# Kernel optimization log

Hardware: AMD Instinct MI355X
Metric: run time of the kernel (lower is better)

Reference implementation:

```python
import jax, jax.numpy as jnp
import numpy as np

D_MODEL = 512
NHEAD = 8
HEAD_DIM = D_MODEL // NHEAD
SEQ = 4096
BATCH = 2
BASE = 10000.0


def rope_cache(seq_len, dim):
    inv_freq = 1.0 / (BASE ** (jnp.arange(0, dim, 2, dtype=jnp.float32) / dim))
    t = jnp.arange(seq_len, dtype=jnp.float32)
    freqs = jnp.einsum('i,j->ij', t, inv_freq)          # [S, dim/2]
    emb = jnp.concatenate([freqs, freqs], axis=-1)       # [S, dim]
    return jnp.cos(emb), jnp.sin(emb)


def rotate_half(x):
    h = x.shape[-1] // 2
    return jnp.concatenate([-x[..., h:], x[..., :h]], axis=-1)


def setup_inputs() -> dict:
    key = jax.random.key(0)
    ks = jax.random.split(key, 9)
    s = 1.0 / np.sqrt(D_MODEL)
    x = jax.random.normal(ks[0], (BATCH, SEQ, D_MODEL), dtype=jnp.float32)
    Wq = jax.random.uniform(ks[1], (D_MODEL, D_MODEL), jnp.float32, -s, s)
    bq = jax.random.uniform(ks[2], (D_MODEL,), jnp.float32, -s, s)
    Wk = jax.random.uniform(ks[3], (D_MODEL, D_MODEL), jnp.float32, -s, s)
    bk = jax.random.uniform(ks[4], (D_MODEL,), jnp.float32, -s, s)
    Wv = jax.random.uniform(ks[5], (D_MODEL, D_MODEL), jnp.float32, -s, s)
    bv = jax.random.uniform(ks[6], (D_MODEL,), jnp.float32, -s, s)
    Wo = jax.random.uniform(ks[7], (D_MODEL, D_MODEL), jnp.float32, -s, s)
    bo = jax.random.uniform(ks[8], (D_MODEL,), jnp.float32, -s, s)
    # causal mask: True where attention is disallowed (j > i)
    mask = jnp.triu(jnp.ones((SEQ, SEQ), dtype=bool), k=1)
    return {"x": x, "mask": mask, "Wq": Wq, "bq": bq, "Wk": Wk, "bk": bk,
            "Wv": Wv, "bv": bv, "Wo": Wo, "bo": bo}


def reference(x, mask, Wq, bq, Wk, bk, Wv, bv, Wo, bo):
    B, S, _ = x.shape
    def proj(W, b):
        y = x @ W.T + b
        return y.reshape(B, S, NHEAD, HEAD_DIM).transpose(0, 2, 1, 3)  # [B,H,S,D]
    q = proj(Wq, bq)
    k = proj(Wk, bk)
    v = proj(Wv, bv)
    cos, sin = rope_cache(S, HEAD_DIM)                    # [S, D]
    cos = cos[None, None]; sin = sin[None, None]
    q = q * cos + rotate_half(q) * sin
    k = k * cos + rotate_half(k) * sin
    scale = HEAD_DIM ** -0.5
    attn = jnp.einsum('bhid,bhjd->bhij', q, k) * scale    # [B,H,S,S]
    attn = jnp.where(mask[None, None], -jnp.inf, attn)
    attn = jax.nn.softmax(attn, axis=-1)
    out = jnp.einsum('bhij,bhjd->bhid', attn, v)          # [B,H,S,D]
    out = out.transpose(0, 2, 1, 3).reshape(B, S, D_MODEL)
    return out @ Wo.T + bo
```

## Files before the change

kernel.cpp:

```cpp
#include <hip/hip_runtime.h>
#include <hip/hip_bf16.h>

#define SEQLEN 4096
#define DMODEL 512
#define NHEADS 8

typedef short short8 __attribute__((ext_vector_type(8)));
typedef float f32x4  __attribute__((ext_vector_type(4)));
typedef float f32x16 __attribute__((ext_vector_type(16)));
typedef int   int2v  __attribute__((ext_vector_type(2)));

__device__ __forceinline__ unsigned short f2bf(float f) {
    union { float f; unsigned u; } v; v.f = f;
    unsigned r = v.u + 0x7fffu + ((v.u >> 16) & 1u);
    return (unsigned short)(r >> 16);
}
__device__ __forceinline__ float bf2f(unsigned short u) {
    union { unsigned u; float f; } v; v.u = (unsigned)u << 16; return v.f;
}
__device__ __forceinline__ float exp2v(float x) {
    float r; asm("v_exp_f32 %0, %1" : "=v"(r) : "v"(x)); return r;
}
__device__ __forceinline__ unsigned cvtpk(float lo, float hi) {
    unsigned r; asm("v_cvt_pk_bf16_f32 %0, %1, %2" : "=v"(r) : "v"(lo), "v"(hi)); return r;
}
__device__ __forceinline__ int2v pl32(int a, int b) {
    return __builtin_amdgcn_permlane32_swap(a, b, false, false);
}
__device__ __forceinline__ void gload16(const void* g, void* l) {
    __builtin_amdgcn_global_load_lds(
        (const __attribute__((address_space(1))) void*)g,
        (__attribute__((address_space(3))) void*)l, 16, 0, 0);
}

__global__ __launch_bounds__(256)
void prep_kernel(const float* __restrict__ x,
                 const float* __restrict__ Wq, const float* __restrict__ Wk,
                 const float* __restrict__ Wv, const float* __restrict__ Wo,
                 unsigned short* __restrict__ xb, unsigned short* __restrict__ Wcat,
                 float* __restrict__ ct, float* __restrict__ st) {
    const int gid = blockIdx.x, tid = threadIdx.x;
    if (gid < 4096) {
        int i = gid * 1024 + tid * 4;
        float4 v = *reinterpret_cast<const float4*>(x + i);
        ushort4 o; o.x = f2bf(v.x); o.y = f2bf(v.y); o.z = f2bf(v.z); o.w = f2bf(v.w);
        *reinterpret_cast<ushort4*>(xb + i) = o;
    } else if (gid < 5120) {
        int i = (gid - 4096) * 1024 + tid * 4;
        int z = i >> 18;
        const float* W = (z == 0) ? Wq : (z == 1) ? Wk : (z == 2) ? Wv : Wo;
        int j = i & 262143;
        float4 v = *reinterpret_cast<const float4*>(W + j);
        ushort4 o; o.x = f2bf(v.x); o.y = f2bf(v.y); o.z = f2bf(v.z); o.w = f2bf(v.w);
        *reinterpret_cast<ushort4*>(Wcat + i) = o;
    } else {
        int idx = (gid - 5120) * 256 + tid;
        int s = idx >> 5, f = idx & 31;
        float inv = powf(10000.0f, -(float)f * (1.0f / 32.0f));
        float a = (float)s * inv;
        ct[idx] = cosf(a); st[idx] = sinf(a);
    }
}

template<int MODE>
__global__ __launch_bounds__(256)
void gemm_kernel(const unsigned short* __restrict__ A,
                 const unsigned short* __restrict__ W,
                 const float* __restrict__ bq,
                 const float* __restrict__ bk,
                 const float* __restrict__ bv,
                 const float* __restrict__ ctab,
                 const float* __restrict__ stab,
                 unsigned short* __restrict__ Qb,
                 unsigned short* __restrict__ Kb,
                 unsigned short* __restrict__ Vt,
                 float* __restrict__ Fout)
{
    constexpr int K = 512;
    constexpr int NT = (MODE == 0) ? 12 : 4;
    constexpr int CPX = (MODE == 0) ? 96 : 32;
    __shared__ __align__(16) unsigned short smem[3][2][128 * 32];

    const int raw = blockIdx.x;
    const int bid = (raw & 7) * CPX + (raw >> 3);
    const int bm = bid / NT, bn = bid % NT;
    const int tid = threadIdx.x;
    const int w = tid >> 6, l = tid & 63;
    const int g = l >> 4, l15 = l & 15;
    const int wr = w >> 1, wc = w & 1;

    const int sr0 = tid >> 2;
    const int swzc = (tid & 3) ^ ((sr0 >> 1) & 3);
    const unsigned wbase = (unsigned)(tid & 0xC0) * 16;
    const unsigned short* arow = A + (size_t)(bm * 128 + sr0) * K + swzc * 8;
    const unsigned short* brow = W + (size_t)(bn * 128 + sr0) * K + swzc * 8;

    f32x4 acc[4][4];
    #pragma unroll
    for (int p = 0; p < 4; ++p)
        #pragma unroll
        for (int q = 0; q < 4; ++q)
            acc[p][q] = (f32x4){0.f, 0.f, 0.f, 0.f};

    auto stage = [&](int buf, int k0) {
        char* ab = (char*)smem[buf][0];
        char* bb2 = (char*)smem[buf][1];
        gload16(arow + k0,                      ab + wbase);
        gload16(arow + (size_t)64 * K + k0,     ab + 4096 + wbase);
        gload16(brow + k0,                      bb2 + wbase);
        gload16(brow + (size_t)64 * K + k0,     bb2 + 4096 + wbase);
    };

    stage(0, 0);
    stage(1, 32);
    asm volatile("s_waitcnt vmcnt(4)" ::: "memory");
    __builtin_amdgcn_s_barrier();

    int cb = 0;
    for (int ks = 0; ks < 16; ++ks) {
        int pb = cb + 2; if (pb >= 3) pb -= 3;
        stage(pb, (ks + 2 < 16) ? (ks + 2) * 32 : 480);

        const char* ab = (const char*)smem[cb][0];
        const char* bb2 = (const char*)smem[cb][1];
        short8 af[4], bf[4];
        #pragma unroll
        for (int mt = 0; mt < 4; ++mt) {
            int r = wr * 64 + mt * 16 + l15;
            int ofs = (r * 64 + g * 16) ^ (((r >> 1) & 3) << 4);
            af[mt] = *reinterpret_cast<const short8*>(ab + ofs);
        }
        #pragma unroll
        for (int nt = 0; nt < 4; ++nt) {
            int r = wc * 64 + nt * 16 + l15;
            int ofs = (r * 64 + g * 16) ^ (((r >> 1) & 3) << 4);
            bf[nt] = *reinterpret_cast<const short8*>(bb2 + ofs);
        }
        __builtin_amdgcn_s_setprio(1);
        #pragma unroll
        for (int mt = 0; mt < 4; ++mt)
            #pragma unroll
            for (int nt = 0; nt < 4; ++nt)
                acc[mt][nt] = __builtin_amdgcn_mfma_f32_16x16x32_bf16(af[mt], bf[nt], acc[mt][nt], 0, 0, 0);
        __builtin_amdgcn_s_setprio(0);

        asm volatile("s_waitcnt vmcnt(4)" ::: "memory");
        __builtin_amdgcn_s_barrier();
        cb = (cb == 2) ? 0 : cb + 1;
    }

    const int m_base = bm * 128 + wr * 64;

    if (MODE == 1) {
        const int n_base = bn * 128 + wc * 64;
        #pragma unroll
        for (int mt = 0; mt < 4; ++mt)
            for (int nt = 0; nt < 4; ++nt) {
                int n = n_base + nt * 16 + l15;
                float bb = bq[n];
                #pragma unroll
                for (int i = 0; i < 4; ++i) {
                    int m = m_base + mt * 16 + g * 4 + i;
                    Fout[(size_t)m * 512 + n] = acc[mt][nt][i] + bb;
                }
            }
    } else {
        const int z = bn >> 2;
        const int nc0 = (bn & 3) * 128 + wc * 64;
        const float* bias = (z == 0) ? bq : (z == 1) ? bk : bv;
        if (z < 2) {
            unsigned short* Y = z ? Kb : Qb;
            const float qsc = z ? 1.0f : 0.18033688011112042f;
            #pragma unroll
            for (int mt = 0; mt < 4; ++mt)
                for (int ntl = 0; ntl < 2; ++ntl) {
                    int hd0 = (ntl * 16 + l15) & 31;
                    int n0 = nc0 + ntl * 16 + l15;
                    float bb0 = bias[n0];
                    float bb1 = bias[n0 + 32];
                    #pragma unroll
                    for (int i = 0; i < 4; ++i) {
                        int m = m_base + mt * 16 + g * 4 + i;
                        int sidx = m & (SEQLEN - 1);
                        float cs = ctab[sidx * 32 + hd0];
                        float sn = stab[sidx * 32 + hd0];
                        float v0 = acc[mt][ntl][i] + bb0;
                        float v1 = acc[mt][ntl + 2][i] + bb1;
                        Y[(size_t)m * 512 + n0]      = f2bf((v0 * cs - v1 * sn) * qsc);
                        Y[(size_t)m * 512 + n0 + 32] = f2bf((v1 * cs + v0 * sn) * qsc);
                    }
                }
        } else {
            asm volatile("s_waitcnt vmcnt(0)" ::: "memory");
            __builtin_amdgcn_s_barrier();
            char* T = (char*)smem;
            #pragma unroll
            for (int mt = 0; mt < 4; ++mt)
                #pragma unroll
                for (int nt = 0; nt < 4; ++nt) {
                    int nv_l = wc * 64 + nt * 16 + l15;
                    float bb = bias[(bn & 3) * 128 + nv_l];
                    #pragma unroll
                    for (int i = 0; i < 4; i += 2) {
                        int m_l = wr * 64 + mt * 16 + g * 4 + i;
                        unsigned u = cvtpk(acc[mt][nt][i] + bb, acc[mt][nt][i + 1] + bb);
                        int byte0 = nv_l * 256 + ((m_l * 2) ^ ((nv_l & 7) << 4));
                        *reinterpret_cast<unsigned*>(T + byte0) = u;
                    }
                }
            __builtin_amdgcn_s_barrier();
            const int b_out = bm >> 5;
            const int s0 = (bm & 31) * 128;
            #pragma unroll
            for (int p = 0; p < 8; ++p) {
                int nv_l = p * 16 + (tid >> 4);
                int c = tid & 15;
                int byte = nv_l * 256 + ((c * 16) ^ ((nv_l & 7) << 4));
                short8 v = *reinterpret_cast<const short8*>(T + byte);
                int nv_g = (bn & 3) * 128 + nv_l;
                int hg = nv_g >> 6, d = nv_g & 63;
                *reinterpret_cast<short8*>(
                    Vt + ((size_t)((b_out * 8 + hg) * 64 + d)) * SEQLEN + s0 + c * 8) = v;
            }
        }
    }
}

template<int SPLIT>
__global__ __launch_bounds__(256, 2)
void attn_kernel(const unsigned short* __restrict__ Qg,
                 const unsigned short* __restrict__ Kg,
                 const unsigned short* __restrict__ Vt,
                 unsigned short* __restrict__ O,
                 unsigned short* __restrict__ Opt,
                 float* __restrict__ Ml)
{
    __shared__ __align__(16) unsigned short k_sh[3][64 * 64];
    __shared__ __align__(16) unsigned short v_sh[3][64 * 64];

    const int bx = blockIdx.x;
    int bh, qsuper, sp;
    if (SPLIT) {
        qsuper = 15 - (bx >> 5);
        bh = (bx >> 1) & 15;
        sp = bx & 1;
    } else {
        qsuper = 15 - (bx >> 4); bh = bx & 15; sp = 0;
    }
    const int HT = 2 * qsuper + 2;
    const int t0 = SPLIT ? sp * HT : 0;
    const int t1 = SPLIT ? t0 + HT : 2 * HT;

    const int b = bh >> 3, hh = bh & 7;
    const int tid = threadIdx.x;
    const int w = tid >> 6, l = tid & 63;
    const int l31 = l & 31, h = l >> 5;

    const size_t qkbase = (size_t)b * SEQLEN * DMODEL + hh * 64;
    const unsigned short* Vrow = Vt + (size_t)bh * 64 * SEQLEN;

    const int r0 = tid >> 3, cb0 = tid & 7;
    const int scs = cb0 ^ (r0 & 7);
    const unsigned short* ksrc0 = Kg + qkbase + (size_t)r0 * DMODEL + scs * 8;
    const unsigned short* vsrc0 = Vrow + (size_t)r0 * SEQLEN + scs * 8;

    const int swz = (l31 & 7) << 4;
    const int td = 4 * qsuper + w;
    const int tlimit = td + 1;
    const int qg0 = qsuper * 256 + w * 64 + l31;
    const int qg1 = qg0 + 32;

    short8 qf0[4], qf1[4];
    {
        const unsigned short* qr0 = Qg + qkbase + (size_t)qg0 * DMODEL;
        const unsigned short* qr1 = Qg + qkbase + (size_t)qg1 * DMODEL;
        #pragma unroll
        for (int kk = 0; kk < 4; ++kk) {
            qf0[kk] = *reinterpret_cast<const short8*>(qr0 + kk * 16 + h * 8);
            qf1[kk] = *reinterpret_cast<const short8*>(qr1 + kk * 16 + h * 8);
        }
    }

    f32x16 oa00, oa01, oa10, oa11;
    #pragma unroll
    for (int i = 0; i < 16; ++i) { oa00[i] = 0.f; oa01[i] = 0.f; oa10[i] = 0.f; oa11[i] = 0.f; }
    float m0 = -3.0e38f, l0 = 0.f, m1 = -3.0e38f, l1 = 0.f;

    auto stage = [&](int buf, int t) {
        char* kb = (char*)k_sh[buf];
        char* vb = (char*)v_sh[buf];
        const unsigned short* kp = ksrc0 + (size_t)t * 64 * DMODEL;
        const unsigned short* vp = vsrc0 + t * 64;
        gload16(kp,                kb + tid * 16);
        gload16(kp + 32 * DMODEL,  kb + 4096 + tid * 16);
        gload16(vp,                vb + tid * 16);
        gload16(vp + 32 * SEQLEN,  vb + 4096 + tid * 16);
    };

    auto softmax_set = [&](f32x16& sA, f32x16& sB, float& mr, float& lr,
                           f32x16& oaA, f32x16& oaB, short8* pw) {
        float mx[16];
        #pragma unroll
        for (int r = 0; r < 16; ++r) mx[r] = fmaxf(sA[r], sB[r]);
        #pragma unroll
        for (int str = 8; str >= 1; str >>= 1)
            #pragma unroll
            for (int r = 0; r < str; ++r) mx[r] = fmaxf(mx[r], mx[r + str]);
        int2v rp2 = pl32(__float_as_int(mx[0]), __float_as_int(mx[0]));
        float pm = fmaxf(__int_as_float(rp2[0]), __int_as_float(rp2[1]));
        float mn = mr;
        if (__any(pm > mr + 8.0f)) {
            mn = fmaxf(mr, pm);
            float al = exp2v(mr - mn);
            mr = mn; lr *= al;
            #pragma unroll
            for (int r = 0; r < 16; ++r) { oaA[r] *= al; oaB[r] *= al; }
        }
        #pragma unroll
        for (int r = 0; r < 16; ++r) sA[r] = exp2v(sA[r] - mn);
        #pragma unroll
        for (int r = 0; r < 16; ++r) sB[r] = exp2v(sB[r] - mn);
        float sm[16];
        #pragma unroll
        for (int r = 0; r < 16; ++r) sm[r] = sA[r] + sB[r];
        #pragma unroll
        for (int str = 8; str >= 1; str >>= 1)
            #pragma unroll
            for (int r = 0; r < str; ++r) sm[r] += sm[r + str];
        int2v rs2 = pl32(__float_as_int(sm[0]), __float_as_int(sm[0]));
        lr += __int_as_float(rs2[0]) + __int_as_float(rs2[1]);
        #pragma unroll
        for (int bb = 0; bb < 4; ++bb) {
            const int rb = (bb & 1) * 8;
            const f32x16& s = (bb < 2) ? sA : sB;
            int pk0 = (int)cvtpk(s[rb + 0], s[rb + 1]);
            int pk1 = (int)cvtpk(s[rb + 2], s[rb + 3]);
            int pk2 = (int)cvtpk(s[rb + 4], s[rb + 5]);
            int pk3 = (int)cvtpk(s[rb + 6], s[rb + 7]);
            int2v r02 = pl32(pk0, pk2);
            int2v r13 = pl32(pk1, pk3);
            union { int u[4]; short8 s8; } w_;
            w_.u[0] = r02[0]; w_.u[1] = r13[0]; w_.u[2] = r02[1]; w_.u[3] = r13[1];
            pw[bb] = w_.s8;
        }
    };

    int cb = t0 % 3;
    stage(cb, t0);
    {
        int nb = cb + 1; if (nb >= 3) nb -= 3;
        stage(nb, (t0 + 1 < t1) ? t0 + 1 : t1 - 1);
    }
    asm volatile("s_waitcnt vmcnt(4)" ::: "memory");
    __builtin_amdgcn_s_barrier();

    for (int t = t0; t < t1; ++t) {
        int pb = cb + 2; if (pb >= 3) pb -= 3;
        stage(pb, (t + 2 < t1) ? t + 2 : t1 - 1);

        if (t < tlimit) {
            const char* kb = (const char*)k_sh[cb];
            const char* vb = (const char*)v_sh[cb];

            f32x16 s00, s01, s10, s11;
            #pragma unroll
            for (int i = 0; i < 16; ++i) { s00[i] = 0.f; s01[i] = 0.f; s10[i] = 0.f; s11[i] = 0.f; }
            __builtin_amdgcn_s_setprio(1);
            #pragma unroll
            for (int kk = 0; kk < 4; ++kk) {
                short8 kf0 = *reinterpret_cast<const short8*>(kb + l31 * 128 + ((kk * 32 + h * 16) ^ swz));
                short8 kf1 = *reinterpret_cast<const short8*>(kb + (32 + l31) * 128 + ((kk * 32 + h * 16) ^ swz));
                s00 = __builtin_amdgcn_mfma_f32_32x32x16_bf16(kf0, qf0[kk], s00, 0, 0, 0);
                s01 = __builtin_amdgcn_mfma_f32_32x32x16_bf16(kf1, qf0[kk], s01, 0, 0, 0);
                s10 = __builtin_amdgcn_mfma_f32_32x32x16_bf16(kf0, qf1[kk], s10, 0, 0, 0);
                s11 = __builtin_amdgcn_mfma_f32_32x32x16_bf16(kf1, qf1[kk], s11, 0, 0, 0);
            }
            __builtin_amdgcn_s_setprio(0);

            if (t == td) {
                #pragma unroll
                for (int r = 0; r < 16; ++r) {
                    int rp = (r & 3) + 8 * (r >> 2) + 4 * h;
                    int kv0 = t * 64 + rp;
                    if (kv0 > qg0)      s00[r] = -3.0e38f;
                    if (kv0 + 32 > qg0) s01[r] = -3.0e38f;
                    if (kv0 > qg1)      s10[r] = -3.0e38f;
                    if (kv0 + 32 > qg1) s11[r] = -3.0e38f;
                }
            }

            short8 pw0[4], pw1[4];
            softmax_set(s00, s01, m0, l0, oa00, oa01, pw0);
            softmax_set(s10, s11, m1, l1, oa10, oa11, pw1);

            __builtin_amdgcn_s_setprio(1);
            #pragma unroll
            for (int bb = 0; bb < 4; ++bb) {
                short8 vf0 = *reinterpret_cast<const short8*>(vb + l31 * 128 + ((bb * 32 + h * 16) ^ swz));
                short8 vf1 = *reinterpret_cast<const short8*>(vb + (32 + l31) * 128 + ((bb * 32 + h * 16) ^ swz));
                oa00 = __builtin_amdgcn_mfma_f32_32x32x16_bf16(vf0, pw0[bb], oa00, 0, 0, 0);
                oa01 = __builtin_amdgcn_mfma_f32_32x32x16_bf16(vf1, pw0[bb], oa01, 0, 0, 0);
                oa10 = __builtin_amdgcn_mfma_f32_32x32x16_bf16(vf0, pw1[bb], oa10, 0, 0, 0);
                oa11 = __builtin_amdgcn_mfma_f32_32x32x16_bf16(vf1, pw1[bb], oa11, 0, 0, 0);
            }
            __builtin_amdgcn_s_setprio(0);
        }

        asm volatile("s_waitcnt vmcnt(4)" ::: "memory");
        __builtin_amdgcn_s_barrier();
        cb = (cb == 2) ? 0 : cb + 1;
    }

    if (SPLIT) {
        float* mlb = Ml + (size_t)(sp * 16 + bh) * 4096 * 2;
        *reinterpret_cast<float2*>(mlb + (size_t)qg0 * 2) = make_float2(m0, l0);
        *reinterpret_cast<float2*>(mlb + (size_t)qg1 * 2) = make_float2(m1, l1);
        unsigned short* opb = Opt + (size_t)(sp * 16 + bh) * 64 * 4096;
        #pragma unroll
        for (int r = 0; r < 16; r += 2) {
            int d0 = (r & 3) + 8 * (r >> 2) + 4 * h;
            unsigned u;
            u = cvtpk(oa00[r], oa00[r + 1]);
            opb[(size_t)d0 * 4096 + qg0] = (unsigned short)u;
            opb[(size_t)(d0 + 1) * 4096 + qg0] = (unsigned short)(u >> 16);
            u = cvtpk(oa01[r], oa01[r + 1]);
            opb[(size_t)(d0 + 32) * 4096 + qg0] = (unsigned short)u;
            opb[(size_t)(d0 + 33) * 4096 + qg0] = (unsigned short)(u >> 16);
            u = cvtpk(oa10[r], oa10[r + 1]);
            opb[(size_t)d0 * 4096 + qg1] = (unsigned short)u;
            opb[(size_t)(d0 + 1) * 4096 + qg1] = (unsigned short)(u >> 16);
            u = cvtpk(oa11[r], oa11[r + 1]);
            opb[(size_t)(d0 + 32) * 4096 + qg1] = (unsigned short)u;
            opb[(size_t)(d0 + 33) * 4096 + qg1] = (unsigned short)(u >> 16);
        }
    } else {
        float inv0 = 1.0f / l0, inv1 = 1.0f / l1;
        unsigned short* or0 = O + qkbase + (size_t)qg0 * DMODEL;
        unsigned short* or1 = O + qkbase + (size_t)qg1 * DMODEL;
        #pragma unroll
        for (int r = 0; r < 16; r += 2) {
            int d0 = (r & 3) + 8 * (r >> 2) + 4 * h;
            *reinterpret_cast<unsigned*>(or0 + d0)      = cvtpk(oa00[r] * inv0, oa00[r + 1] * inv0);
            *reinterpret_cast<unsigned*>(or0 + 32 + d0) = cvtpk(oa01[r] * inv0, oa01[r + 1] * inv0);
            *reinterpret_cast<unsigned*>(or1 + d0)      = cvtpk(oa10[r] * inv1, oa10[r + 1] * inv1);
            *reinterpret_cast<unsigned*>(or1 + 32 + d0) = cvtpk(oa11[r] * inv1, oa11[r + 1] * inv1);
        }
    }
}

__global__ __launch_bounds__(256)
void combine_kernel(const unsigned short* __restrict__ Opt, const float* __restrict__ Ml,
                    unsigned short* __restrict__ O) {
    __shared__ float a0_sh[64], a1_sh[64];
    __shared__ unsigned short o_sh[64][72];
    const int bx = blockIdx.x;
    const int bh = bx >> 6, qt = bx & 63;
    const int b = bh >> 3, hh = bh & 7;
    const int q0 = qt * 64;
    const int tid = threadIdx.x;

    if (tid < 64) {
        int q = q0 + tid;
        float2 ml0 = *reinterpret_cast<const float2*>(Ml + ((size_t)bh * 4096 + q) * 2);
        float2 ml1 = *reinterpret_cast<const float2*>(Ml + ((size_t)(16 + bh) * 4096 + q) * 2);
        float m = fmaxf(ml0.x, ml1.x);
        float a0 = exp2v(ml0.x - m), a1 = exp2v(ml1.x - m);
        float inv = 1.0f / (a0 * ml0.y + a1 * ml1.y);
        a0_sh[tid] = a0 * inv;
        a1_sh[tid] = a1 * inv;
    }
    __syncthreads();

    const int d = tid >> 2, q4 = (tid & 3) * 16;
    const unsigned short* p0 = Opt + ((size_t)bh * 64 + d) * 4096 + q0 + q4;
    const unsigned short* p1 = Opt + ((size_t)(16 + bh) * 64 + d) * 4096 + q0 + q4;
    #pragma unroll
    for (int j = 0; j < 16; j += 8) {
        short8 v0 = *reinterpret_cast<const short8*>(p0 + j);
        short8 v1 = *reinterpret_cast<const short8*>(p1 + j);
        #pragma unroll
        for (int e = 0; e < 8; ++e) {
            int q = q4 + j + e;
            o_sh[q][d] = f2bf(a0_sh[q] * bf2f((unsigned short)v0[e]) +
                              a1_sh[q] * bf2f((unsigned short)v1[e]));
        }
    }
    __syncthreads();

    const int qw = tid >> 2, dc = (tid & 3) * 16;
    unsigned short* orow = O + ((size_t)(b * 4096 + q0 + qw)) * 512 + hh * 64 + dc;
    #pragma unroll
    for (int j = 0; j < 2; ++j) {
        union { ushort4 h4[2]; short8 s8; } u;
        u.h4[0] = *reinterpret_cast<const ushort4*>(&o_sh[qw][dc + j * 8]);
        u.h4[1] = *reinterpret_cast<const ushort4*>(&o_sh[qw][dc + j * 8 + 4]);
        *reinterpret_cast<short8*>(orow + j * 8) = u.s8;
    }
}

extern "C" void kernel_launch(void* const* d_in, const int* in_sizes, int n_in,
                              void* d_out, int out_size, void* d_ws, size_t ws_size,
                              hipStream_t stream) {
    const float* x  = (const float*)d_in[0];
    const float* Wq = (const float*)d_in[2];
    const float* bq = (const float*)d_in[3];
    const float* Wk = (const float*)d_in[4];
    const float* bk = (const float*)d_in[5];
    const float* Wv = (const float*)d_in[6];
    const float* bv = (const float*)d_in[7];
    const float* Wo = (const float*)d_in[8];
    const float* bo = (const float*)d_in[9];
    float* out = (float*)d_out;

    const int MD = 8192 * 512;
    const int WD = 512 * 512;
    unsigned short* ws  = (unsigned short*)d_ws;
    unsigned short* xb  = ws;
    unsigned short* Qb  = xb + MD;
    unsigned short* Kb  = Qb + MD;
    unsigned short* Vt  = Kb + MD;
    unsigned short* Ob  = Vt + MD;
    unsigned short* Wcat = Ob + MD;
    float* ctab = (float*)(Wcat + 4 * WD);
    float* stab = ctab + SEQLEN * 32;
    unsigned short* Opt = (unsigned short*)((char*)d_ws + 45088768ull);
    float* Ml  = (float*)((char*)d_ws + 78643200ull);
    const size_t NEED = 79691776ull;
    const bool split = (ws_size >= NEED);

    prep_kernel<<<5632, 256, 0, stream>>>(x, Wq, Wk, Wv, Wo, xb, Wcat, ctab, stab);

    gemm_kernel<0><<<dim3(64 * 12), 256, 0, stream>>>(
        xb, Wcat, bq, bk, bv, ctab, stab, Qb, Kb, Vt, nullptr);

    if (split) {
        attn_kernel<1><<<dim3(512), 256, 0, stream>>>(Qb, Kb, Vt, nullptr, Opt, Ml);
        combine_kernel<<<dim3(1024), 256, 0, stream>>>(Opt, Ml, Ob);
    } else {
        attn_kernel<0><<<dim3(256), 256, 0, stream>>>(Qb, Kb, Vt, Ob, nullptr, nullptr);
    }

    gemm_kernel<1><<<dim3(64 * 4), 256, 0, stream>>>(
        Ob, Wcat + 3 * WD, bo, nullptr, nullptr, nullptr, nullptr,
        nullptr, nullptr, nullptr, out);
}
```

Measured before the change: 227.0 us.

## Split attention KV range into fixed-size chunks for balanced causal scheduling

Replaces the fixed two-way KV split per query super-tile with a variable number of chunks of ten KV tiles each. The split count now grows with the causal row length, giving 976 work items of similar size instead of 512 uneven ones. Short rows that fit in one chunk write normalized output directly, and longer rows write partial outputs plus max and sum values that a generalized combine kernel merges across up to seven chunks. The fallback path now also uses the split buffers, so it relies on the workspace being large enough, and it costs more partial-output traffic.

After: 221.7 us. -2.3%, faster.

```diff
diff --git a/kernel.cpp b/kernel.cpp
--- a/kernel.cpp
+++ b/kernel.cpp
@@ -32,6 +32,7 @@
         (const __attribute__((address_space(1))) void*)g,
         (__attribute__((address_space(3))) void*)l, 16, 0, 0);
 }
+__device__ __forceinline__ int nchunks(int qs) { return (4 * qs + 4 + 9) / 10; }
 
 __global__ __launch_bounds__(256)
 void prep_kernel(const float* __restrict__ x,
@@ -226,7 +227,6 @@
     }
 }
 
-template<int SPLIT>
 __global__ __launch_bounds__(256, 2)
 void attn_kernel(const unsigned short* __restrict__ Qg,
                  const unsigned short* __restrict__ Kg,
@@ -239,17 +239,20 @@
     __shared__ __align__(16) unsigned short v_sh[3][64 * 64];
 
     const int bx = blockIdx.x;
-    int bh, qsuper, sp;
-    if (SPLIT) {
-        qsuper = 15 - (bx >> 5);
-        bh = (bx >> 1) & 15;
-        sp = bx & 1;
-    } else {
-        qsuper = 15 - (bx >> 4); bh = bx & 15; sp = 0;
-    }
-    const int HT = 2 * qsuper + 2;
-    const int t0 = SPLIT ? sp * HT : 0;
-    const int t1 = SPLIT ? t0 + HT : 2 * HT;
+    const int bh = bx & 15;
+    const int idx = bx >> 4;
+    int qs = 15, accn = 0;
+    for (;;) {
+        int nb = nchunks(qs);
+        if (accn + nb > idx) break;
+        accn += nb; --qs;
+    }
+    const int ck = idx - accn;
+    const int HT4 = 4 * qs + 4;
+    const int t0 = ck * 10;
+    const int t1 = (t0 + 10 < HT4) ? t0 + 10 : HT4;
+    const bool single = (HT4 <= 10);
+    const int slot = bh * 61 + idx;
 
     const int b = bh >> 3, hh = bh & 7;
     const int tid = threadIdx.x;
@@ -265,10 +268,12 @@
     const unsigned short* vsrc0 = Vrow + (size_t)r0 * SEQLEN + scs * 8;
 
     const int swz = (l31 & 7) << 4;
-    const int td = 4 * qsuper + w;
+    const int td = 4 * qs + w;
     const int tlimit = td + 1;
-    const int qg0 = qsuper * 256 + w * 64 + l31;
+    const int qg0 = qs * 256 + w * 64 + l31;
     const int qg1 = qg0 + 32;
+    const int ql0 = w * 64 + l31;
+    const int ql1 = ql0 + 32;
 
     short8 qf0[4], qf1[4];
     {
@@ -411,29 +416,7 @@
         cb = (cb == 2) ? 0 : cb + 1;
     }
 
-    if (SPLIT) {
-        float* mlb = Ml + (size_t)(sp * 16 + bh) * 4096 * 2;
-        *reinterpret_cast<float2*>(mlb + (size_t)qg0 * 2) = make_float2(m0, l0);
-        *reinterpret_cast<float2*>(mlb + (size_t)qg1 * 2) = make_float2(m1, l1);
-        unsigned short* opb = Opt + (size_t)(sp * 16 + bh) * 64 * 4096;
-        #pragma unroll
-        for (int r = 0; r < 16; r += 2) {
-            int d0 = (r & 3) + 8 * (r >> 2) + 4 * h;
-            unsigned u;
-            u = cvtpk(oa00[r], oa00[r + 1]);
-            opb[(size_t)d0 * 4096 + qg0] = (unsigned short)u;
-            opb[(size_t)(d0 + 1) * 4096 + qg0] = (unsigned short)(u >> 16);
-            u = cvtpk(oa01[r], oa01[r + 1]);
-            opb[(size_t)(d0 + 32) * 4096 + qg0] = (unsigned short)u;
-            opb[(size_t)(d0 + 33) * 4096 + qg0] = (unsigned short)(u >> 16);
-            u = cvtpk(oa10[r], oa10[r + 1]);
-            opb[(size_t)d0 * 4096 + qg1] = (unsigned short)u;
-            opb[(size_t)(d0 + 1) * 4096 + qg1] = (unsigned short)(u >> 16);
-            u = cvtpk(oa11[r], oa11[r + 1]);
-            opb[(size_t)(d0 + 32) * 4096 + qg1] = (unsigned short)u;
-            opb[(size_t)(d0 + 33) * 4096 + qg1] = (unsigned short)(u >> 16);
-        }
-    } else {
+    if (single) {
         float inv0 = 1.0f / l0, inv1 = 1.0f / l1;
         unsigned short* or0 = O + qkbase + (size_t)qg0 * DMODEL;
         unsigned short* or1 = O + qkbase + (size_t)qg1 * DMODEL;
@@ -445,50 +428,86 @@
             *reinterpret_cast<unsigned*>(or1 + d0)      = cvtpk(oa10[r] * inv1, oa10[r + 1] * inv1);
             *reinterpret_cast<unsigned*>(or1 + 32 + d0) = cvtpk(oa11[r] * inv1, oa11[r + 1] * inv1);
         }
+    } else {
+        float* mlb = Ml + (size_t)slot * 512;
+        *reinterpret_cast<float2*>(mlb + ql0 * 2) = make_float2(m0, l0);
+        *reinterpret_cast<float2*>(mlb + ql1 * 2) = make_float2(m1, l1);
+        unsigned short* opb = Opt + (size_t)slot * 16384;
+        #pragma unroll
+        for (int r = 0; r < 16; r += 2) {
+            int d0 = (r & 3) + 8 * (r >> 2) + 4 * h;
+            unsigned u;
+            u = cvtpk(oa00[r], oa00[r + 1]);
+            opb[d0 * 256 + ql0]        = (unsigned short)u;
+            opb[(d0 + 1) * 256 + ql0]  = (unsigned short)(u >> 16);
+            u = cvtpk(oa01[r], oa01[r + 1]);
+            opb[(d0 + 32) * 256 + ql0] = (unsigned short)u;
+            opb[(d0 + 33) * 256 + ql0] = (unsigned short)(u >> 16);
+            u = cvtpk(oa10[r], oa10[r + 1]);
+            opb[d0 * 256 + ql1]        = (unsigned short)u;
+            opb[(d0 + 1) * 256 + ql1]  = (unsigned short)(u >> 16);
+            u = cvtpk(oa11[r], oa11[r + 1]);
+            opb[(d0 + 32) * 256 + ql1] = (unsigned short)u;
+            opb[(d0 + 33) * 256 + ql1] = (unsigned short)(u >> 16);
+        }
     }
 }
 
 __global__ __launch_bounds__(256)
 void combine_kernel(const unsigned short* __restrict__ Opt, const float* __restrict__ Ml,
                     unsigned short* __restrict__ O) {
-    __shared__ float a0_sh[64], a1_sh[64];
+    __shared__ float a_sh[7][64];
     __shared__ unsigned short o_sh[64][72];
     const int bx = blockIdx.x;
-    const int bh = bx >> 6, qt = bx & 63;
+    const int qs = 2 + (bx >> 6);
+    const int rem = bx & 63;
+    const int bh = rem >> 2, qq = rem & 3;
     const int b = bh >> 3, hh = bh & 7;
-    const int q0 = qt * 64;
     const int tid = threadIdx.x;
 
+    int accn = 0;
+    for (int q2 = 15; q2 > qs; --q2) accn += nchunks(q2);
+    const int nb = nchunks(qs);
+    const int slotbase = bh * 61 + accn;
+
     if (tid < 64) {
-        int q = q0 + tid;
-        float2 ml0 = *reinterpret_cast<const float2*>(Ml + ((size_t)bh * 4096 + q) * 2);
-        float2 ml1 = *reinterpret_cast<const float2*>(Ml + ((size_t)(16 + bh) * 4096 + q) * 2);
-        float m = fmaxf(ml0.x, ml1.x);
-        float a0 = exp2v(ml0.x - m), a1 = exp2v(ml1.x - m);
-        float inv = 1.0f / (a0 * ml0.y + a1 * ml1.y);
-        a0_sh[tid] = a0 * inv;
-        a1_sh[tid] = a1 * inv;
+        int q = qq * 64 + tid;
+        float m = -3.0e38f;
+        for (int c = 0; c < nb; ++c)
+            m = fmaxf(m, Ml[(size_t)(slotbase + c) * 512 + q * 2]);
+        float denom = 0.f;
+        for (int c = 0; c < nb; ++c) {
+            float2 ml = *reinterpret_cast<const float2*>(Ml + (size_t)(slotbase + c) * 512 + q * 2);
+            float a = exp2v(ml.x - m);
+            denom += a * ml.y;
+            a_sh[c][tid] = a;
+        }
+        float inv = 1.0f / denom;
+        for (int c = 0; c < nb; ++c) a_sh[c][tid] *= inv;
     }
     __syncthreads();
 
     const int d = tid >> 2, q4 = (tid & 3) * 16;
-    const unsigned short* p0 = Opt + ((size_t)bh * 64 + d) * 4096 + q0 + q4;
-    const unsigned short* p1 = Opt + ((size_t)(16 + bh) * 64 + d) * 4096 + q0 + q4;
+    float acc16[16];
     #pragma unroll
-    for (int j = 0; j < 16; j += 8) {
-        short8 v0 = *reinterpret_cast<const short8*>(p0 + j);
-        short8 v1 = *reinterpret_cast<const short8*>(p1 + j);
+    for (int e = 0; e < 16; ++e) acc16[e] = 0.f;
+    for (int c = 0; c < nb; ++c) {
+        const unsigned short* p = Opt + (size_t)(slotbase + c) * 16384 + d * 256 + qq * 64 + q4;
+        short8 v0 = *reinterpret_cast<const short8*>(p);
+        short8 v1 = *reinterpret_cast<const short8*>(p + 8);
         #pragma unroll
         for (int e = 0; e < 8; ++e) {
-            int q = q4 + j + e;
-            o_sh[q][d] = f2bf(a0_sh[q] * bf2f((unsigned short)v0[e]) +
-                              a1_sh[q] * bf2f((unsigned short)v1[e]));
-        }
-    }
+            acc16[e]     += a_sh[c][q4 + e]     * bf2f((unsigned short)v0[e]);
+            acc16[8 + e] += a_sh[c][q4 + 8 + e] * bf2f((unsigned short)v1[e]);
+        }
+    }
+    #pragma unroll
+    for (int e = 0; e < 16; ++e) o_sh[q4 + e][d] = f2bf(acc16[e]);
     __syncthreads();
 
     const int qw = tid >> 2, dc = (tid & 3) * 16;
-    unsigned short* orow = O + ((size_t)(b * 4096 + q0 + qw)) * 512 + hh * 64 + dc;
+    const int qglob = qs * 256 + qq * 64 + qw;
+    unsigned short* orow = O + ((size_t)(b * 4096 + qglob)) * 512 + hh * 64 + dc;
     #pragma unroll
     for (int j = 0; j < 2; ++j) {
         union { ushort4 h4[2]; short8 s8; } u;
@@ -524,7 +543,7 @@
     float* ctab = (float*)(Wcat + 4 * WD);
     float* stab = ctab + SEQLEN * 32;
     unsigned short* Opt = (unsigned short*)((char*)d_ws + 45088768ull);
-    float* Ml  = (float*)((char*)d_ws + 78643200ull);
+    float* Ml  = (float*)((char*)d_ws + 45088768ull + 31981568ull);
     const size_t NEED = 79691776ull;
     const bool split = (ws_size >= NEED);
 
@@ -534,10 +553,11 @@
         xb, Wcat, bq, bk, bv, ctab, stab, Qb, Kb, Vt, nullptr);
 
     if (split) {
-        attn_kernel<1><<<dim3(512), 256, 0, stream>>>(Qb, Kb, Vt, nullptr, Opt, Ml);
-        combine_kernel<<<dim3(1024), 256, 0, stream>>>(Opt, Ml, Ob);
+        attn_kernel<<<dim3(976), 256, 0, stream>>>(Qb, Kb, Vt, Ob, Opt, Ml);
+        combine_kernel<<<dim3(896), 256, 0, stream>>>(Opt, Ml, Ob);
     } else {
-        attn_kernel<0><<<dim3(256), 256, 0, stream>>>(Qb, Kb, Vt, Ob, nullptr, nullptr);
+        attn_kernel<<<dim3(976), 256, 0, stream>>>(Qb, Kb, Vt, Ob, Opt, Ml);
+        combine_kernel<<<dim3(896), 256, 0, stream>>>(Opt, Ml, Ob);
     }
 
     gemm_kernel<1><<<dim3(64 * 4), 256, 0, stream>>>(
```
